# Optimization experiments

Measured on AMD Instinct MI355X. Metric: run time of the kernel, lower is better.

The kernel has to match this reference:

```python
import jax, jax.numpy as jnp
import numpy as np

B, S, D, H = 1, 4096, 1024, 16
DH = D // H  # 64
SCALE = D ** 0.5  # original divides by input_dim**0.5, not head_dim**0.5


def setup_inputs() -> dict:
    key = jax.random.key(0)
    ks = jax.random.split(key, 11)
    s = lambda i, shape, sc=1.0: jax.random.normal(ks[i], shape, dtype=jnp.float32) * sc
    w_init = 1.0 / np.sqrt(D)
    return {
        "q": s(0, (B, S, D)),
        "k": s(1, (B, S, D)),
        "v": s(2, (B, S, D)),
        "Wq": s(3, (H, D, DH), w_init),
        "bq": jnp.zeros((H, DH), jnp.float32),
        "Wk": s(4, (H, D, DH), w_init),
        "bk": jnp.zeros((H, DH), jnp.float32),
        "Wv": s(5, (H, D, DH), w_init),
        "bv": jnp.zeros((H, DH), jnp.float32),
        "Wo": s(6, (D, D), w_init),
        "bo": jnp.zeros((D,), jnp.float32),
    }


def reference(q, k, v, Wq, bq, Wk, bk, Wv, bv, Wo, bo):
    # Per-head Dense projections, batched over heads: [B,S,D] x [H,D,dh] -> [B,H,S,dh]
    Q = jnp.einsum("bsd,hde->bhse", q, Wq) + bq[None, :, None, :]
    K = jnp.einsum("bsd,hde->bhse", k, Wk) + bk[None, :, None, :]
    V = jnp.einsum("bsd,hde->bhse", v, Wv) + bv[None, :, None, :]
    # Scaled dot-product attention; note scale = sqrt(input_dim) as in source
    scores = jnp.einsum("bhse,bhte->bhst", Q, K) / SCALE  # [B,H,S,S]
    attn = jax.nn.softmax(scores, axis=-1)
    out = jnp.einsum("bhst,bhte->bhse", attn, V)  # [B,H,S,dh]
    # Concat heads along feature dim (head order matches the Python loop)
    concat = out.transpose(0, 2, 1, 3).reshape(q.shape[0], q.shape[1], H * DH)
    return concat @ Wo + bo
```

## Files before the change

### kernel.cpp

```cpp
#include <hip/hip_runtime.h>
#include <hip/hip_bf16.h>

#define S_LEN 4096
#define D_MODEL 1024
#define NH 16
#define DHEAD 64
#define QSCALE 0.0450843293f

typedef __attribute__((ext_vector_type(8))) short short8;
typedef __attribute__((ext_vector_type(4))) float floatx4;

__device__ __forceinline__ unsigned short f2bf(float f) {
    unsigned int x = __float_as_uint(f);
    x += 0x7fffu + ((x >> 16) & 1u);
    return (unsigned short)(x >> 16);
}

__device__ __forceinline__ float exp2_fast(float x) {
    return __builtin_amdgcn_exp2f(x);
}

__device__ __forceinline__ void async_copy16(const unsigned short* g, unsigned short* l) {
    __builtin_amdgcn_global_load_lds(
        (const __attribute__((address_space(1))) void*)g,
        (__attribute__((address_space(3))) void*)l, 16, 0, 0);
}

__global__ __launch_bounds__(256) void prep_cast(
    const float* __restrict__ q, const float* __restrict__ k,
    const float* __restrict__ v, unsigned short* __restrict__ dst)
{
    long i = (long)(blockIdx.x * 256 + threadIdx.x) * 8;
    int which = (int)(i >> 22);
    long off = i & ((1 << 22) - 1);
    const float* src = (which == 0) ? q : (which == 1) ? k : v;
    float4 f0 = *(const float4*)&src[off];
    float4 f1 = *(const float4*)&src[off + 4];
    uint4 o;
    o.x = (unsigned int)f2bf(f0.x) | ((unsigned int)f2bf(f0.y) << 16);
    o.y = (unsigned int)f2bf(f0.z) | ((unsigned int)f2bf(f0.w) << 16);
    o.z = (unsigned int)f2bf(f1.x) | ((unsigned int)f2bf(f1.y) << 16);
    o.w = (unsigned int)f2bf(f1.z) | ((unsigned int)f2bf(f1.w) << 16);
    *(uint4*)&dst[i] = o;
}

__global__ __launch_bounds__(256) void prep_transpose(
    const float* __restrict__ Wq, const float* __restrict__ Wk,
    const float* __restrict__ Wv, const float* __restrict__ Wo,
    unsigned short* __restrict__ ws)
{
    __shared__ float L[64][65];
    const int bx  = blockIdx.x;
    const int mat = bx >> 8;
    const int tid = threadIdx.x;

    if (mat < 3) {
        const float* W = (mat == 0) ? Wq : (mat == 1) ? Wk : Wv;
        unsigned short* WT = ws + (size_t)mat * (1u << 20);
        int h  = (bx >> 4) & 15;
        int dt = bx & 15;
        #pragma unroll
        for (int i = 0; i < 16; i++) {
            int idx = i * 256 + tid;
            int dp = idx >> 6, e = idx & 63;
            L[e][dp] = W[h * 65536 + (dt * 64 + dp) * 64 + e];
        }
        __syncthreads();
        #pragma unroll
        for (int i = 0; i < 16; i++) {
            int idx = i * 256 + tid;
            int e = idx >> 6, dp = idx & 63;
            WT[(h * 64 + e) * 1024 + dt * 64 + dp] = f2bf(L[e][dp]);
        }
    } else {
        unsigned short* WoT = ws + (size_t)3 * (1u << 20);
        int rt = (bx >> 4) & 15;
        int ct = bx & 15;
        #pragma unroll
        for (int i = 0; i < 16; i++) {
            int idx = i * 256 + tid;
            int dp = idx >> 6, np = idx & 63;
            L[np][dp] = Wo[(rt * 64 + dp) * 1024 + ct * 64 + np];
        }
        __syncthreads();
        #pragma unroll
        for (int i = 0; i < 16; i++) {
            int idx = i * 256 + tid;
            int np = idx >> 6, dp = idx & 63;
            WoT[(ct * 64 + np) * 1024 + rt * 64 + dp] = f2bf(L[np][dp]);
        }
    }
}

#define GEMM_CORE(XPTR, WPTR)                                                   \
    for (int k0 = 0; k0 < D_MODEL; k0 += 64) {                                  \
        __syncthreads();                                                        \
        _Pragma("unroll")                                                       \
        for (int i = 0; i < 4; i++) {                                           \
            async_copy16(&XPTR[(size_t)(m0 + srow + i * 8) * D_MODEL + k0 + scol], \
                         &As[(wave * 32 + i * 8) * 64]);                        \
            async_copy16(&WPTR[(size_t)(n0 + srow + i * 8) * D_MODEL + k0 + scol], \
                         &Bs[(wave * 32 + i * 8) * 64]);                        \
        }                                                                       \
        __syncthreads();                                                        \
        _Pragma("unroll")                                                       \
        for (int ks = 0; ks < 2; ks++) {                                        \
            short8 af[4], bf[4];                                                \
            _Pragma("unroll")                                                   \
            for (int i = 0; i < 4; i++)                                         \
                af[i] = *(const short8*)&As[(wr * 64 + i * 16 + m) * 64 + ks * 32 + quad * 8]; \
            _Pragma("unroll")                                                   \
            for (int j = 0; j < 4; j++)                                         \
                bf[j] = *(const short8*)&Bs[(wc * 64 + j * 16 + m) * 64 + ks * 32 + quad * 8]; \
            _Pragma("unroll")                                                   \
            for (int i = 0; i < 4; i++) {                                       \
                _Pragma("unroll")                                               \
                for (int j = 0; j < 4; j++)                                     \
                    acc[i][j] = __builtin_amdgcn_mfma_f32_16x16x32_bf16(af[i], bf[j], acc[i][j], 0, 0, 0); \
            }                                                                   \
        }                                                                       \
    }

__global__ __launch_bounds__(256) void qkv_gemm(
    const unsigned short* __restrict__ Xbase, const unsigned short* __restrict__ WTbase,
    const float* __restrict__ bq, const float* __restrict__ bk,
    const float* __restrict__ bv,
    unsigned short* __restrict__ Qbuf, unsigned short* __restrict__ Kbuf,
    unsigned short* __restrict__ Vbuf)
{
    __shared__ __align__(16) unsigned short As[128 * 64];
    __shared__ __align__(16) unsigned short Bs[128 * 64];

    const int z = blockIdx.z;
    const unsigned short* X  = Xbase + (size_t)z * (4u << 20);
    const unsigned short* WT = WTbase + (size_t)z * (1u << 20);
    const float* bias = (z == 0) ? bq : (z == 1) ? bk : bv;

    const int n0 = blockIdx.x * 128;
    const int m0 = blockIdx.y * 128;
    const int tid = threadIdx.x, wave = tid >> 6, lane = tid & 63;
    const int m = lane & 15, quad = lane >> 4;
    const int wr = wave >> 1, wc = wave & 1;
    const int srow = wave * 32 + (lane >> 3);
    const int scol = (lane & 7) * 8;

    floatx4 acc[4][4];
    #pragma unroll
    for (int i = 0; i < 4; i++)
        #pragma unroll
        for (int j = 0; j < 4; j++) acc[i][j] = (floatx4){0.f, 0.f, 0.f, 0.f};

    GEMM_CORE(X, WT)

    #pragma unroll
    for (int j = 0; j < 4; j++) {
        int n = n0 + wc * 64 + j * 16 + m;
        int h = n >> 6, e = n & 63;
        float bvv = bias[n];
        #pragma unroll
        for (int i = 0; i < 4; i++) {
            int sbase = m0 + wr * 64 + i * 16 + quad * 4;
            if (z == 2) {
                ushort4 pk;
                pk.x = f2bf(acc[i][j][0] + bvv);
                pk.y = f2bf(acc[i][j][1] + bvv);
                pk.z = f2bf(acc[i][j][2] + bvv);
                pk.w = f2bf(acc[i][j][3] + bvv);
                *(ushort4*)&Vbuf[h * (DHEAD * S_LEN) + e * S_LEN + sbase] = pk;
            } else if (z == 1) {
                #pragma unroll
                for (int r = 0; r < 4; r++)
                    Kbuf[h * (S_LEN * DHEAD) + (sbase + r) * DHEAD + e] = f2bf(acc[i][j][r] + bvv);
            } else {
                #pragma unroll
                for (int r = 0; r < 4; r++)
                    Qbuf[h * (S_LEN * DHEAD) + (sbase + r) * DHEAD + e] =
                        f2bf((acc[i][j][r] + bvv) * QSCALE);
            }
        }
    }
}

__global__ __launch_bounds__(256) void out_gemm(
    const unsigned short* __restrict__ Cbuf, const unsigned short* __restrict__ WoT,
    const float* __restrict__ bo, float* __restrict__ out)
{
    __shared__ __align__(16) unsigned short As[128 * 64];
    __shared__ __align__(16) unsigned short Bs[128 * 64];

    const int n0 = blockIdx.x * 128;
    const int m0 = blockIdx.y * 128;
    const int tid = threadIdx.x, wave = tid >> 6, lane = tid & 63;
    const int m = lane & 15, quad = lane >> 4;
    const int wr = wave >> 1, wc = wave & 1;
    const int srow = wave * 32 + (lane >> 3);
    const int scol = (lane & 7) * 8;

    floatx4 acc[4][4];
    #pragma unroll
    for (int i = 0; i < 4; i++)
        #pragma unroll
        for (int j = 0; j < 4; j++) acc[i][j] = (floatx4){0.f, 0.f, 0.f, 0.f};

    GEMM_CORE(Cbuf, WoT)

    #pragma unroll
    for (int j = 0; j < 4; j++) {
        int n = n0 + wc * 64 + j * 16 + m;
        float bvv = bo[n];
        #pragma unroll
        for (int i = 0; i < 4; i++) {
            int sbase = m0 + wr * 64 + i * 16 + quad * 4;
            #pragma unroll
            for (int r = 0; r < 4; r++)
                out[(size_t)(sbase + r) * D_MODEL + n] = acc[i][j][r] + bvv;
        }
    }
}

__global__ __launch_bounds__(256) void attn_kernel(
    const unsigned short* __restrict__ Q, const unsigned short* __restrict__ K,
    const unsigned short* __restrict__ VT, unsigned short* __restrict__ concat)
{
    __shared__ __align__(16) unsigned char ldsraw[40960];
    unsigned short* lds16 = (unsigned short*)ldsraw;

    const int h  = blockIdx.y;
    const int q0 = blockIdx.x * 64;
    const unsigned short* Qh = Q  + h * (S_LEN * DHEAD);
    const unsigned short* Kh = K  + h * (S_LEN * DHEAD);
    const unsigned short* Vh = VT + h * (DHEAD * S_LEN);

    const int tid  = threadIdx.x;
    const int wave = tid >> 6;
    const int lane = tid & 63;
    const int m    = lane & 15;
    const int quad = lane >> 4;
    const int swz  = (m & 7) << 3;
    const int lrow = lane >> 3;
    const int lcol = ((lane & 7) * 8) ^ (lrow << 3);

    unsigned short* Ps = lds16 + 16384;

    #pragma unroll
    for (int i = 0; i < 2; i++) {
        int c = 2 * wave + i;
        async_copy16(&Qh[(size_t)(q0 + 8 * c + lrow) * DHEAD + lcol], Ps + c * 512);
        async_copy16(&Kh[(size_t)(8 * c + lrow) * DHEAD + lcol], lds16 + c * 512);
        async_copy16(&Vh[(size_t)(8 * c + lrow) * S_LEN + lcol], lds16 + 8192 + c * 512);
    }
    asm volatile("s_waitcnt vmcnt(0)" ::: "memory");
    __builtin_amdgcn_s_barrier();

    short8 bq[4][2];
    #pragma unroll
    for (int qc = 0; qc < 4; qc++)
        #pragma unroll
        for (int ks = 0; ks < 2; ks++)
            bq[qc][ks] = *(const short8*)&Ps[(qc * 16 + m) * 64 + ((ks * 32 + quad * 8) ^ swz)];
    __syncthreads();

    floatx4 O[4];
    #pragma unroll
    for (int nb = 0; nb < 4; nb++) O[nb] = (floatx4){0.f, 0.f, 0.f, 0.f};
    float lsum[4] = {0.f, 0.f, 0.f, 0.f};

    for (int t0 = 0; t0 < S_LEN; t0 += 64) {
        const int cur = (t0 >> 6) & 1;
        unsigned short* Ksc = lds16 + cur * 4096;
        unsigned short* Vsc = lds16 + 8192 + cur * 4096;

        if (t0) {
            asm volatile("s_waitcnt vmcnt(0)" ::: "memory");
            __builtin_amdgcn_s_barrier();
        }
        if (t0 + 64 < S_LEN) {
            unsigned short* Ksn = lds16 + (cur ^ 1) * 4096;
            unsigned short* Vsn = lds16 + 8192 + (cur ^ 1) * 4096;
            #pragma unroll
            for (int i = 0; i < 2; i++) {
                int c = 2 * wave + i;
                async_copy16(&Kh[(size_t)(t0 + 64 + 8 * c + lrow) * DHEAD + lcol],
                             Ksn + c * 512);
                async_copy16(&Vh[(size_t)(8 * c + lrow) * S_LEN + t0 + 64 + lcol],
                             Vsn + c * 512);
            }
        }

        floatx4 st[4];
        #pragma unroll
        for (int qc = 0; qc < 4; qc++) st[qc] = (floatx4){0.f, 0.f, 0.f, 0.f};
        #pragma unroll
        for (int ks = 0; ks < 2; ks++) {
            short8 a = *(const short8*)&Ksc[(wave * 16 + m) * 64 + ((ks * 32 + quad * 8) ^ swz)];
            __builtin_amdgcn_s_setprio(1);
            #pragma unroll
            for (int qc = 0; qc < 4; qc++)
                st[qc] = __builtin_amdgcn_mfma_f32_16x16x32_bf16(a, bq[qc][ks], st[qc], 0, 0, 0);
            __builtin_amdgcn_s_setprio(0);
        }

        #pragma unroll
        for (int qc = 0; qc < 4; qc++) {
            float p0 = exp2_fast(st[qc][0]);
            float p1 = exp2_fast(st[qc][1]);
            float p2 = exp2_fast(st[qc][2]);
            float p3 = exp2_fast(st[qc][3]);
            lsum[qc] += (p0 + p1) + (p2 + p3);
            unsigned u0 = __float_as_uint(p0) + 0x8000u;
            unsigned u1 = __float_as_uint(p1) + 0x8000u;
            unsigned u2 = __float_as_uint(p2) + 0x8000u;
            unsigned u3 = __float_as_uint(p3) + 0x8000u;
            uint2 pk;
            pk.x = __builtin_amdgcn_perm(u1, u0, 0x07060302u);
            pk.y = __builtin_amdgcn_perm(u3, u2, 0x07060302u);
            *(uint2*)&Ps[(qc * 16 + m) * 64 + ((wave * 16 + quad * 4) ^ swz)] = pk;
        }
        asm volatile("s_waitcnt lgkmcnt(0)" ::: "memory");
        __builtin_amdgcn_s_barrier();

        #pragma unroll
        for (int ks = 0; ks < 2; ks++) {
            short8 ap = *(const short8*)&Ps[(wave * 16 + m) * 64 + ((ks * 32 + quad * 8) ^ swz)];
            __builtin_amdgcn_s_setprio(1);
            #pragma unroll
            for (int nb = 0; nb < 4; nb++) {
                short8 bv = *(const short8*)&Vsc[(nb * 16 + m) * 64 + ((ks * 32 + quad * 8) ^ swz)];
                O[nb] = __builtin_amdgcn_mfma_f32_16x16x32_bf16(ap, bv, O[nb], 0, 0, 0);
            }
            __builtin_amdgcn_s_setprio(0);
        }
    }

    #pragma unroll
    for (int qc = 0; qc < 4; qc++) {
        lsum[qc] += __shfl_xor(lsum[qc], 16);
        lsum[qc] += __shfl_xor(lsum[qc], 32);
    }
    float* Ls = (float*)ldsraw;
    if (quad == 0) {
        #pragma unroll
        for (int qc = 0; qc < 4; qc++) Ls[wave * 64 + qc * 16 + m] = lsum[qc];
    }
    __syncthreads();
    float linv[4];
    #pragma unroll
    for (int r = 0; r < 4; r++) {
        int qq = wave * 16 + quad * 4 + r;
        linv[r] = 1.0f / (Ls[0 * 64 + qq] + Ls[1 * 64 + qq] + Ls[2 * 64 + qq] + Ls[3 * 64 + qq]);
    }

    #pragma unroll
    for (int nb = 0; nb < 4; nb++) {
        int e = nb * 16 + m;
        #pragma unroll
        for (int r = 0; r < 4; r++) {
            int s = q0 + wave * 16 + quad * 4 + r;
            concat[s * D_MODEL + h * DHEAD + e] = f2bf(O[nb][r] * linv[r]);
        }
    }
}

extern "C" void kernel_launch(void* const* d_in, const int* in_sizes, int n_in,
                              void* d_out, int out_size, void* d_ws, size_t ws_size,
                              hipStream_t stream) {
    const float* q  = (const float*)d_in[0];
    const float* k  = (const float*)d_in[1];
    const float* v  = (const float*)d_in[2];
    const float* Wq = (const float*)d_in[3];
    const float* bq = (const float*)d_in[4];
    const float* Wk = (const float*)d_in[5];
    const float* bk = (const float*)d_in[6];
    const float* Wv = (const float*)d_in[7];
    const float* bv = (const float*)d_in[8];
    const float* Wo = (const float*)d_in[9];
    const float* bo = (const float*)d_in[10];
    float* out = (float*)d_out;

    unsigned short* ws = (unsigned short*)d_ws;
    const size_t M1 = 1u << 20;
    unsigned short* WqT  = ws;
    unsigned short* WoT  = ws + 3 * M1;
    unsigned short* Qbuf = ws + 4 * M1;
    unsigned short* Kbuf = ws + 8 * M1;
    unsigned short* Vbuf = ws + 12 * M1;
    unsigned short* Cbuf = ws + 16 * M1;
    unsigned short* qb   = ws + 20 * M1;

    prep_cast<<<6144, 256, 0, stream>>>(q, k, v, qb);
    prep_transpose<<<1024, 256, 0, stream>>>(Wq, Wk, Wv, Wo, ws);

    dim3 gq(8, 32, 3);
    qkv_gemm<<<gq, 256, 0, stream>>>(qb, WqT, bq, bk, bv, Qbuf, Kbuf, Vbuf);

    dim3 ga(64, 16);
    attn_kernel<<<ga, 256, 0, stream>>>(Qbuf, Kbuf, Vbuf, Cbuf);

    dim3 gg(8, 32);
    out_gemm<<<gg, 256, 0, stream>>>(Cbuf, WoT, bo, out);
}
```

Before: 300.2 us.

## Merge prep kernels, double attention query tile per block, use packed bf16 convert

The two preprocessing kernels become one launch that branches on block index, saving a launch. The attention kernel now runs 512 threads over 128 queries per block: eight waves split into four key-row groups and two query halves. Each 64-key K/V tile loaded into LDS now serves twice as many queries, halving K/V traffic per query, at the cost of larger LDS use and half as many blocks (512 instead of 1024). The manual round-and-perm bf16 packing of probabilities is replaced by the hardware v_cvt_pk_bf16_f32 instruction, which may round slightly differently.

```diff
diff --git a/kernel.cpp b/kernel.cpp
--- a/kernel.cpp
+++ b/kernel.cpp
@@ -26,33 +26,34 @@
         (__attribute__((address_space(3))) void*)l, 16, 0, 0);
 }
 
-__global__ __launch_bounds__(256) void prep_cast(
+__global__ __launch_bounds__(256) void prep_all(
     const float* __restrict__ q, const float* __restrict__ k,
-    const float* __restrict__ v, unsigned short* __restrict__ dst)
-{
-    long i = (long)(blockIdx.x * 256 + threadIdx.x) * 8;
-    int which = (int)(i >> 22);
-    long off = i & ((1 << 22) - 1);
-    const float* src = (which == 0) ? q : (which == 1) ? k : v;
-    float4 f0 = *(const float4*)&src[off];
-    float4 f1 = *(const float4*)&src[off + 4];
-    uint4 o;
-    o.x = (unsigned int)f2bf(f0.x) | ((unsigned int)f2bf(f0.y) << 16);
-    o.y = (unsigned int)f2bf(f0.z) | ((unsigned int)f2bf(f0.w) << 16);
-    o.z = (unsigned int)f2bf(f1.x) | ((unsigned int)f2bf(f1.y) << 16);
-    o.w = (unsigned int)f2bf(f1.z) | ((unsigned int)f2bf(f1.w) << 16);
-    *(uint4*)&dst[i] = o;
-}
-
-__global__ __launch_bounds__(256) void prep_transpose(
+    const float* __restrict__ v,
     const float* __restrict__ Wq, const float* __restrict__ Wk,
     const float* __restrict__ Wv, const float* __restrict__ Wo,
-    unsigned short* __restrict__ ws)
+    unsigned short* __restrict__ dst, unsigned short* __restrict__ ws)
 {
     __shared__ float L[64][65];
-    const int bx  = blockIdx.x;
+    const int tid = threadIdx.x;
+
+    if (blockIdx.x < 6144) {
+        long i = (long)(blockIdx.x * 256 + tid) * 8;
+        int which = (int)(i >> 22);
+        long off = i & ((1 << 22) - 1);
+        const float* src = (which == 0) ? q : (which == 1) ? k : v;
+        float4 f0 = *(const float4*)&src[off];
+        float4 f1 = *(const float4*)&src[off + 4];
+        uint4 o;
+        o.x = (unsigned int)f2bf(f0.x) | ((unsigned int)f2bf(f0.y) << 16);
+        o.y = (unsigned int)f2bf(f0.z) | ((unsigned int)f2bf(f0.w) << 16);
+        o.z = (unsigned int)f2bf(f1.x) | ((unsigned int)f2bf(f1.y) << 16);
+        o.w = (unsigned int)f2bf(f1.z) | ((unsigned int)f2bf(f1.w) << 16);
+        *(uint4*)&dst[i] = o;
+        return;
+    }
+
+    const int bx  = blockIdx.x - 6144;
     const int mat = bx >> 8;
-    const int tid = threadIdx.x;
 
     if (mat < 3) {
         const float* W = (mat == 0) ? Wq : (mat == 1) ? Wk : Wv;
@@ -218,21 +219,23 @@
     }
 }
 
-__global__ __launch_bounds__(256) void attn_kernel(
+__global__ __launch_bounds__(512) void attn_kernel(
     const unsigned short* __restrict__ Q, const unsigned short* __restrict__ K,
     const unsigned short* __restrict__ VT, unsigned short* __restrict__ concat)
 {
-    __shared__ __align__(16) unsigned char ldsraw[40960];
+    __shared__ __align__(16) unsigned char ldsraw[49152];
     unsigned short* lds16 = (unsigned short*)ldsraw;
 
     const int h  = blockIdx.y;
-    const int q0 = blockIdx.x * 64;
+    const int q0 = blockIdx.x * 128;
     const unsigned short* Qh = Q  + h * (S_LEN * DHEAD);
     const unsigned short* Kh = K  + h * (S_LEN * DHEAD);
     const unsigned short* Vh = VT + h * (DHEAD * S_LEN);
 
     const int tid  = threadIdx.x;
     const int wave = tid >> 6;
+    const int wt   = wave & 3;
+    const int wq   = wave >> 2;
     const int lane = tid & 63;
     const int m    = lane & 15;
     const int quad = lane >> 4;
@@ -246,9 +249,9 @@
     for (int i = 0; i < 2; i++) {
         int c = 2 * wave + i;
         async_copy16(&Qh[(size_t)(q0 + 8 * c + lrow) * DHEAD + lcol], Ps + c * 512);
-        async_copy16(&Kh[(size_t)(8 * c + lrow) * DHEAD + lcol], lds16 + c * 512);
-        async_copy16(&Vh[(size_t)(8 * c + lrow) * S_LEN + lcol], lds16 + 8192 + c * 512);
-    }
+    }
+    async_copy16(&Kh[(size_t)(8 * wave + lrow) * DHEAD + lcol], lds16 + wave * 512);
+    async_copy16(&Vh[(size_t)(8 * wave + lrow) * S_LEN + lcol], lds16 + 8192 + wave * 512);
     asm volatile("s_waitcnt vmcnt(0)" ::: "memory");
     __builtin_amdgcn_s_barrier();
 
@@ -257,7 +260,7 @@
     for (int qc = 0; qc < 4; qc++)
         #pragma unroll
         for (int ks = 0; ks < 2; ks++)
-            bq[qc][ks] = *(const short8*)&Ps[(qc * 16 + m) * 64 + ((ks * 32 + quad * 8) ^ swz)];
+            bq[qc][ks] = *(const short8*)&Ps[(wq * 64 + qc * 16 + m) * 64 + ((ks * 32 + quad * 8) ^ swz)];
     __syncthreads();
 
     floatx4 O[4];
@@ -277,14 +280,10 @@
         if (t0 + 64 < S_LEN) {
             unsigned short* Ksn = lds16 + (cur ^ 1) * 4096;
             unsigned short* Vsn = lds16 + 8192 + (cur ^ 1) * 4096;
-            #pragma unroll
-            for (int i = 0; i < 2; i++) {
-                int c = 2 * wave + i;
-                async_copy16(&Kh[(size_t)(t0 + 64 + 8 * c + lrow) * DHEAD + lcol],
-                             Ksn + c * 512);
-                async_copy16(&Vh[(size_t)(8 * c + lrow) * S_LEN + t0 + 64 + lcol],
-                             Vsn + c * 512);
-            }
+            async_copy16(&Kh[(size_t)(t0 + 64 + 8 * wave + lrow) * DHEAD + lcol],
+                         Ksn + wave * 512);
+            async_copy16(&Vh[(size_t)(8 * wave + lrow) * S_LEN + t0 + 64 + lcol],
+                         Vsn + wave * 512);
         }
 
         floatx4 st[4];
@@ -292,7 +291,7 @@
         for (int qc = 0; qc < 4; qc++) st[qc] = (floatx4){0.f, 0.f, 0.f, 0.f};
         #pragma unroll
         for (int ks = 0; ks < 2; ks++) {
-            short8 a = *(const short8*)&Ksc[(wave * 16 + m) * 64 + ((ks * 32 + quad * 8) ^ swz)];
+            short8 a = *(const short8*)&Ksc[(wt * 16 + m) * 64 + ((ks * 32 + quad * 8) ^ swz)];
             __builtin_amdgcn_s_setprio(1);
             #pragma unroll
             for (int qc = 0; qc < 4; qc++)
@@ -307,14 +306,13 @@
             float p2 = exp2_fast(st[qc][2]);
             float p3 = exp2_fast(st[qc][3]);
             lsum[qc] += (p0 + p1) + (p2 + p3);
-            unsigned u0 = __float_as_uint(p0) + 0x8000u;
-            unsigned u1 = __float_as_uint(p1) + 0x8000u;
-            unsigned u2 = __float_as_uint(p2) + 0x8000u;
-            unsigned u3 = __float_as_uint(p3) + 0x8000u;
+            unsigned r0, r1;
+            asm("v_cvt_pk_bf16_f32 %0, %1, %2" : "=v"(r0) : "v"(p0), "v"(p1));
+            asm("v_cvt_pk_bf16_f32 %0, %1, %2" : "=v"(r1) : "v"(p2), "v"(p3));
             uint2 pk;
-            pk.x = __builtin_amdgcn_perm(u1, u0, 0x07060302u);
-            pk.y = __builtin_amdgcn_perm(u3, u2, 0x07060302u);
-            *(uint2*)&Ps[(qc * 16 + m) * 64 + ((wave * 16 + quad * 4) ^ swz)] = pk;
+            pk.x = r0;
+            pk.y = r1;
+            *(uint2*)&Ps[(wq * 64 + qc * 16 + m) * 64 + ((wt * 16 + quad * 4) ^ swz)] = pk;
         }
         asm volatile("s_waitcnt lgkmcnt(0)" ::: "memory");
         __builtin_amdgcn_s_barrier();
@@ -340,14 +338,16 @@
     float* Ls = (float*)ldsraw;
     if (quad == 0) {
         #pragma unroll
-        for (int qc = 0; qc < 4; qc++) Ls[wave * 64 + qc * 16 + m] = lsum[qc];
+        for (int qc = 0; qc < 4; qc++)
+            Ls[wt * 128 + wq * 64 + qc * 16 + m] = lsum[qc];
     }
     __syncthreads();
     float linv[4];
     #pragma unroll
     for (int r = 0; r < 4; r++) {
         int qq = wave * 16 + quad * 4 + r;
-        linv[r] = 1.0f / (Ls[0 * 64 + qq] + Ls[1 * 64 + qq] + Ls[2 * 64 + qq] + Ls[3 * 64 + qq]);
+        linv[r] = 1.0f / (Ls[0 * 128 + qq] + Ls[1 * 128 + qq] +
+                          Ls[2 * 128 + qq] + Ls[3 * 128 + qq]);
     }
 
     #pragma unroll
@@ -387,14 +387,13 @@
     unsigned short* Cbuf = ws + 16 * M1;
     unsigned short* qb   = ws + 20 * M1;
 
-    prep_cast<<<6144, 256, 0, stream>>>(q, k, v, qb);
-    prep_transpose<<<1024, 256, 0, stream>>>(Wq, Wk, Wv, Wo, ws);
+    prep_all<<<7168, 256, 0, stream>>>(q, k, v, Wq, Wk, Wv, Wo, qb, ws);
 
     dim3 gq(8, 32, 3);
     qkv_gemm<<<gq, 256, 0, stream>>>(qb, WqT, bq, bk, bv, Qbuf, Kbuf, Vbuf);
 
-    dim3 ga(64, 16);
-    attn_kernel<<<ga, 256, 0, stream>>>(Qbuf, Kbuf, Vbuf, Cbuf);
+    dim3 ga(32, 16);
+    attn_kernel<<<ga, 512, 0, stream>>>(Qbuf, Kbuf, Vbuf, Cbuf);
 
     dim3 gg(8, 32);
     out_gemm<<<gg, 256, 0, stream>>>(Cbuf, WoT, bo, out);
```

After: 272.5 us. -9.2%, faster.
